# Optimization experiments

Measured on AMD Instinct MI355X. Metric: run time of the kernel, lower is better.

## Reference

```python
import jax, jax.numpy as jnp
import numpy as np

EPS = 1e-12  # torch F.normalize default eps

def _l2norm(x):
    # F.normalize(x, dim=1): x / max(||x||, eps)
    n = jnp.sqrt(jnp.sum(x * x, axis=1, keepdims=True))
    return x / jnp.maximum(n, EPS)

def setup_inputs() -> dict:
    key = jax.random.key(0)
    k1, k2 = jax.random.split(key)
    B, M, D = 4096, 8192, 1024
    query = jax.random.normal(k1, (B, D), dtype=jnp.float32)
    memory = jax.random.normal(k2, (M, D), dtype=jnp.float32)
    return {"query": query, "memory": memory}

def reference(query, memory):
    # memory buffer is normalized at construction time
    mem = _l2norm(memory)              # [M, D]
    q = _l2norm(query)                 # [B, D]
    sim = jnp.einsum('bd,md->bm', q, mem)          # [B, M] cosine similarity
    attn = jax.nn.softmax(sim, axis=1)             # [B, M]
    memory_features = jnp.einsum('bm,md->bd', attn, mem)  # [B, D]
    return (memory_features, attn)
```

## Files before the change

### kernel.cpp

```cpp
#include <hip/hip_runtime.h>
#include <stdint.h>

#define NB 4096
#define NM 8192
#define ND 1024

typedef __attribute__((ext_vector_type(8))) short bf16x8;
typedef __attribute__((ext_vector_type(4))) float f32x4;
typedef __attribute__((ext_vector_type(8))) unsigned short u16x8;

static __device__ __forceinline__ unsigned short f2bf(float f) {
  union { float f; uint32_t u; } v; v.f = f;
  uint32_t u = v.u;
  u += 0x7fffu + ((u >> 16) & 1u);
  return (unsigned short)(u >> 16);
}
static __device__ __forceinline__ float bf2f(unsigned short b) {
  union { uint32_t u; float f; } v; v.u = ((uint32_t)b) << 16; return v.f;
}

static __device__ __forceinline__ void gload_lds16(const void* g, void* l) {
  __builtin_amdgcn_global_load_lds(
      (__attribute__((address_space(1))) void*)g,
      (__attribute__((address_space(3))) void*)l, 16, 0, 0);
}

#define BAR()   __builtin_amdgcn_s_barrier()
#define LGKM0() asm volatile("s_waitcnt lgkmcnt(0)" ::: "memory")
#define VMC8()  asm volatile("s_waitcnt vmcnt(8)" ::: "memory")
#define VMC2()  asm volatile("s_waitcnt vmcnt(2)" ::: "memory")
#define VMC0()  asm volatile("s_waitcnt vmcnt(0)" ::: "memory")

__global__ void nrm_kernel(const float* __restrict__ x, unsigned short* __restrict__ out) {
  const int row = blockIdx.x, t = threadIdx.x;
  const float4 v = ((const float4*)(x + (size_t)row * ND))[t];
  float ss = v.x * v.x + v.y * v.y + v.z * v.z + v.w * v.w;
  #pragma unroll
  for (int o = 32; o > 0; o >>= 1) ss += __shfl_xor(ss, o);
  __shared__ float red[4];
  if ((t & 63) == 0) red[t >> 6] = ss;
  __syncthreads();
  ss = (red[0] + red[1]) + (red[2] + red[3]);
  const float sc = 1.0f / fmaxf(sqrtf(ss), 1e-12f);
  ushort4 o4;
  o4.x = f2bf(v.x * sc); o4.y = f2bf(v.y * sc);
  o4.z = f2bf(v.z * sc); o4.w = f2bf(v.w * sc);
  ((ushort4*)(out + (size_t)row * ND))[t] = o4;
}

__global__ void tr_kernel(const unsigned short* __restrict__ memn, unsigned short* __restrict__ memt) {
  __shared__ unsigned short Ts[64][66];
  const int t = threadIdx.x;
  const int d0 = blockIdx.x * 64, m0 = blockIdx.y * 64;
  #pragma unroll
  for (int r = 0; r < 2; ++r) {
    const int lrow = r * 32 + (t >> 3);
    const int lcol = (t & 7) * 8;
    u16x8 v = *(const u16x8*)(memn + (size_t)(m0 + lrow) * ND + d0 + lcol);
    #pragma unroll
    for (int j = 0; j < 8; ++j) Ts[lcol + j][lrow] = v[j];
  }
  __syncthreads();
  #pragma unroll
  for (int r = 0; r < 2; ++r) {
    const int orow = r * 32 + (t >> 3);
    const int ocol = (t & 7) * 8;
    u16x8 o;
    #pragma unroll
    for (int j = 0; j < 8; ++j) o[j] = Ts[orow][ocol + j];
    *(u16x8*)(memt + (size_t)(d0 + orow) * NM + m0 + ocol) = o;
  }
}

template<int MODE>
__global__ __launch_bounds__(512, 2) void gemm4r(
    const unsigned short* __restrict__ A, const unsigned short* __restrict__ B,
    void* __restrict__ Cv, float* __restrict__ psum,
    int ld, int ldc, int mt, int tps, int kchunk, unsigned long long cstride)
{
  extern __shared__ char smem[];
  const int t = threadIdx.x;
  const int w = t >> 6, l = t & 63;
  const int wr = w >> 2, wc = w & 3;
  const int nwg = gridDim.x, cpx = nwg >> 3;
  const int id = (blockIdx.x & 7) * cpx + (blockIdx.x >> 3);
  const int ksp = id / tps, rem = id % tps;
  const int brow = rem % mt, bcol = rem / mt;
  const int k0 = ksp * kchunk;
  const int nt = kchunk >> 6;

  const int srow = l >> 3;
  const int scol = ((l & 7) ^ srow) << 3;
  const int lr = l & 15, lhi = l >> 4;
  const int swz = (l & 7) << 4;
  const int cbk0 = (lhi * 16) ^ swz;
  const int cbk1 = (64 + lhi * 16) ^ swz;
  const int aoffr = (wr * 16 + lr) * 128;
  const int boffr = (wc * 16 + lr) * 128;

  const unsigned short* Ab = A + (size_t)(brow * 256 + w * 8 + srow) * ld + k0 + scol;
  const unsigned short* Bb = B + (size_t)(bcol * 256 + w * 8 + srow) * ld + k0 + scol;

  auto stageA = [&](int p, int h, int tau) {
    const int kt = (tau < nt ? tau : nt - 1) << 6;
    const unsigned short* g = Ab + (size_t)(h * 128) * ld + kt;
    char* d = smem + p * 65536 + h * 16384 + w * 1024;
    gload_lds16(g, d);
    gload_lds16(g + (size_t)64 * ld, d + 8192);
  };
  auto stageB = [&](int p, int h, int tau) {
    const int kt = (tau < nt ? tau : nt - 1) << 6;
    const unsigned short* g = Bb + (size_t)(h * 128) * ld + kt;
    char* d = smem + p * 65536 + 32768 + h * 16384 + w * 1024;
    gload_lds16(g, d);
    gload_lds16(g + (size_t)64 * ld, d + 8192);
  };
  auto ldA = [&](int p, int m, int kk) -> bf16x8 {
    return *(const bf16x8*)(smem + p * 65536 + m * 4096 + aoffr + (kk ? cbk1 : cbk0));
  };
  auto ldB = [&](int p, int nf, int kk) -> bf16x8 {
    return *(const bf16x8*)(smem + p * 65536 + 32768 + nf * 8192 + boffr + (kk ? cbk1 : cbk0));
  };

  f32x4 acc[8][4] = {};
  bf16x8 alo[4][2], ahi[4][2], bloA[2][2], bloB[2][2], bhi[2][2];

  stageA(0, 0, 0); stageA(0, 1, 0); stageB(0, 0, 0); stageB(0, 1, 0);
  stageA(1, 0, 1); stageA(1, 1, 1); stageB(1, 0, 1); stageB(1, 1, 1);
  VMC8();
  BAR();
  #pragma unroll
  for (int m = 0; m < 4; ++m) { alo[m][0] = ldA(0, m, 0); alo[m][1] = ldA(0, m, 1); }
  #pragma unroll
  for (int n = 0; n < 2; ++n) { bloA[n][0] = ldB(0, n, 0); bloA[n][1] = ldB(0, n, 1); }

  #define CL(AF, BF, MO, NO)                                                   \
    __builtin_amdgcn_s_setprio(1);                                             \
    _Pragma("unroll")                                                          \
    for (int kk = 0; kk < 2; ++kk)                                             \
      _Pragma("unroll")                                                        \
      for (int m = 0; m < 4; ++m)                                              \
        _Pragma("unroll")                                                      \
        for (int n = 0; n < 2; ++n)                                            \
          acc[MO + m][NO + n] = __builtin_amdgcn_mfma_f32_16x16x32_bf16(       \
              AF[m][kk], BF[n][kk], acc[MO + m][NO + n], 0, 0, 0);             \
    __builtin_amdgcn_s_setprio(0);

  const int niter = nt >> 1;
  for (int i = 0; i < niter; ++i) {
    const int t2 = 2 * i + 2, t3 = 2 * i + 3;
    LGKM0();
    CL(alo, bloA, 0, 0);
    #pragma unroll
    for (int n = 0; n < 2; ++n) { bhi[n][0] = ldB(0, 2 + n, 0); bhi[n][1] = ldB(0, 2 + n, 1); }
    BAR();
    LGKM0();
    CL(alo, bhi, 0, 2);
    #pragma unroll
    for (int m = 0; m < 4; ++m) { ahi[m][0] = ldA(0, 4 + m, 0); ahi[m][1] = ldA(0, 4 + m, 1); }
    stageB(0, 0, t2);
    VMC2();
    BAR();
    LGKM0();
    CL(ahi, bhi, 4, 2);
    #pragma unroll
    for (int n = 0; n < 2; ++n) { bloB[n][0] = ldB(1, n, 0); bloB[n][1] = ldB(1, n, 1); }
    stageB(0, 1, t2); stageA(0, 0, t2);
    BAR();
    LGKM0();
    CL(ahi, bloA, 4, 0);
    #pragma unroll
    for (int m = 0; m < 4; ++m) { alo[m][0] = ldA(1, m, 0); alo[m][1] = ldA(1, m, 1); }
    stageA(0, 1, t2);
    BAR();
    LGKM0();
    CL(alo, bloB, 0, 0);
    #pragma unroll
    for (int n = 0; n < 2; ++n) { bhi[n][0] = ldB(1, 2 + n, 0); bhi[n][1] = ldB(1, 2 + n, 1); }
    BAR();
    LGKM0();
    CL(alo, bhi, 0, 2);
    #pragma unroll
    for (int m = 0; m < 4; ++m) { ahi[m][0] = ldA(1, 4 + m, 0); ahi[m][1] = ldA(1, 4 + m, 1); }
    stageB(1, 0, t3);
    VMC2();
    BAR();
    LGKM0();
    CL(ahi, bhi, 4, 2);
    #pragma unroll
    for (int n = 0; n < 2; ++n) { bloA[n][0] = ldB(0, n, 0); bloA[n][1] = ldB(0, n, 1); }
    stageB(1, 1, t3); stageA(1, 0, t3);
    BAR();
    LGKM0();
    CL(ahi, bloB, 4, 0);
    #pragma unroll
    for (int m = 0; m < 4; ++m) { alo[m][0] = ldA(0, m, 0); alo[m][1] = ldA(0, m, 1); }
    stageA(1, 1, t3);
    BAR();
  }
  #undef CL

  const int crow0 = brow * 256 + wr * 16 + lhi * 4;
  const int ccol0 = bcol * 256 + wc * 16 + lr;
  if constexpr (MODE == 1) {
    unsigned short* Cp = (unsigned short*)Cv;
    float rs[8][4];
    #pragma unroll
    for (int m = 0; m < 8; ++m)
      #pragma unroll
      for (int j = 0; j < 4; ++j) rs[m][j] = 0.f;
    #pragma unroll
    for (int m = 0; m < 8; ++m)
      #pragma unroll
      for (int n = 0; n < 4; ++n)
        #pragma unroll
        for (int j = 0; j < 4; ++j) {
          const float e = __expf(acc[m][n][j]);
          rs[m][j] += e;
          Cp[(size_t)(crow0 + m * 32 + j) * ldc + ccol0 + n * 64] = f2bf(e);
        }
    #pragma unroll
    for (int m = 0; m < 8; ++m)
      #pragma unroll
      for (int j = 0; j < 4; ++j)
        #pragma unroll
        for (int o = 1; o < 16; o <<= 1) rs[m][j] += __shfl_xor(rs[m][j], o);
    VMC0();
    __syncthreads();
    float* ls = (float*)smem;
    if (lr == 0) {
      #pragma unroll
      for (int m = 0; m < 8; ++m)
        #pragma unroll
        for (int j = 0; j < 4; ++j)
          ls[wc * 256 + wr * 16 + m * 32 + lhi * 4 + j] = rs[m][j];
    }
    __syncthreads();
    if (t < 256) {
      const float s4 = ls[t] + ls[256 + t] + ls[512 + t] + ls[768 + t];
      psum[(size_t)bcol * NB + brow * 256 + t] = s4;
    }
  } else {
    float* Cp = (float*)Cv + (unsigned long long)ksp * cstride;
    #pragma unroll
    for (int m = 0; m < 8; ++m)
      #pragma unroll
      for (int n = 0; n < 4; ++n)
        #pragma unroll
        for (int j = 0; j < 4; ++j)
          Cp[(size_t)(crow0 + m * 32 + j) * ldc + ccol0 + n * 64] = acc[m][n][j];
  }
}

__global__ void scale_kernel(const unsigned short* __restrict__ E,
                             const float* __restrict__ psum,
                             float* __restrict__ attn, float* __restrict__ sinv) {
  const int row = blockIdx.x, t = threadIdx.x;
  __shared__ float sh;
  if (t < 64) {
    float p = (t < 32) ? psum[(size_t)t * NB + row] : 0.f;
    #pragma unroll
    for (int o = 16; o > 0; o >>= 1) p += __shfl_xor(p, o);
    if (t == 0) { sh = p; sinv[row] = 1.0f / p; }
  }
  __syncthreads();
  const float inv = 1.0f / sh;
  const unsigned short* erow = E + (size_t)row * NM;
  float* arow = attn + (size_t)row * NM;
  #pragma unroll
  for (int i = 0; i < 4; ++i) {
    u16x8 bv = ((const u16x8*)erow)[i * 256 + t];
    float4 f0, f1;
    #pragma unroll
    for (int j = 0; j < 8; ++j) {
      const float a = bf2f(bv[j]) * inv;
      if (j < 4) (&f0.x)[j] = a; else (&f1.x)[j - 4] = a;
    }
    const int e = (i * 256 + t) * 8;
    *(float4*)(arow + e) = f0;
    *(float4*)(arow + e + 4) = f1;
  }
}

__global__ void reduce_kernel(const float4* __restrict__ part, float4* __restrict__ mf,
                              const float* __restrict__ sinv) {
  const size_t n4 = (size_t)NB * ND / 4;
  for (size_t i = (size_t)blockIdx.x * blockDim.x + threadIdx.x; i < n4;
       i += (size_t)gridDim.x * blockDim.x) {
    const float is = sinv[i >> 8];
    float4 s = part[i];
    #pragma unroll
    for (int k = 1; k < 4; ++k) {
      float4 p = part[(size_t)k * n4 + i];
      s.x += p.x; s.y += p.y; s.z += p.z; s.w += p.w;
    }
    s.x *= is; s.y *= is; s.z *= is; s.w *= is;
    mf[i] = s;
  }
}

extern "C" void kernel_launch(void* const* d_in, const int* in_sizes, int n_in,
                              void* d_out, int out_size, void* d_ws, size_t ws_size,
                              hipStream_t stream) {
  const float* q   = (const float*)d_in[0];
  const float* mem = (const float*)d_in[1];
  float* mf   = (float*)d_out;
  float* attn = (float*)d_out + (size_t)NB * ND;
  char* ws = (char*)d_ws;
  unsigned short* qn   = (unsigned short*)(ws);
  unsigned short* memn = (unsigned short*)(ws + ((size_t)8  << 20));
  unsigned short* memt = (unsigned short*)(ws + ((size_t)24 << 20));
  unsigned short* E    = (unsigned short*)(ws + ((size_t)40 << 20));
  float* psum          = (float*)(ws + ((size_t)104 << 20));
  float* sinv          = (float*)(ws + ((size_t)104 << 20) + (512 << 10));
  float* part          = (float*)(ws + ((size_t)105 << 20));

  hipFuncSetAttribute((const void*)gemm4r<1>,
                      hipFuncAttributeMaxDynamicSharedMemorySize, 131072);
  hipFuncSetAttribute((const void*)gemm4r<0>,
                      hipFuncAttributeMaxDynamicSharedMemorySize, 131072);

  hipLaunchKernelGGL(nrm_kernel, dim3(NM), dim3(256), 0, stream, mem, memn);
  hipLaunchKernelGGL(nrm_kernel, dim3(NB), dim3(256), 0, stream, q, qn);
  hipLaunchKernelGGL(tr_kernel, dim3(ND / 64, NM / 64), dim3(256), 0, stream, memn, memt);

  hipLaunchKernelGGL((gemm4r<1>), dim3((NB / 256) * (NM / 256)), dim3(512), 131072, stream,
                     qn, memn, (void*)E, psum, ND, NM, NB / 256,
                     (NB / 256) * (NM / 256), ND, 0ULL);

  hipLaunchKernelGGL(scale_kernel, dim3(NB), dim3(256), 0, stream, E, psum, attn, sinv);

  const int tps = (NB / 256) * (ND / 256);
  hipLaunchKernelGGL((gemm4r<0>), dim3(tps * 4), dim3(512), 131072, stream,
                     E, memt, (void*)part, (float*)nullptr, NM, ND, NB / 256, tps, NM / 4,
                     (unsigned long long)NB * ND);
  hipLaunchKernelGGL(reduce_kernel, dim3(2048), dim3(256), 0, stream,
                     (const float4*)part, (float4*)mf, sinv);
}
```

Measured before the change: 208.3 us.

## Fuse attn scaling into second GEMM epilogue and restructure GEMM pipeline per tile

```diff
diff --git a/kernel.cpp b/kernel.cpp
--- a/kernel.cpp
+++ b/kernel.cpp
@@ -27,8 +27,8 @@
 
 #define BAR()   __builtin_amdgcn_s_barrier()
 #define LGKM0() asm volatile("s_waitcnt lgkmcnt(0)" ::: "memory")
-#define VMC8()  asm volatile("s_waitcnt vmcnt(8)" ::: "memory")
-#define VMC2()  asm volatile("s_waitcnt vmcnt(2)" ::: "memory")
+#define LGKM8() asm volatile("s_waitcnt lgkmcnt(8)" ::: "memory")
+#define VMC4()  asm volatile("s_waitcnt vmcnt(4)" ::: "memory")
 #define VMC0()  asm volatile("s_waitcnt vmcnt(0)" ::: "memory")
 
 __global__ void nrm_kernel(const float* __restrict__ x, unsigned short* __restrict__ out) {
@@ -73,9 +73,10 @@
 }
 
 template<int MODE>
-__global__ __launch_bounds__(512, 2) void gemm4r(
+__global__ __launch_bounds__(512, 2) void gemmht(
     const unsigned short* __restrict__ A, const unsigned short* __restrict__ B,
     void* __restrict__ Cv, float* __restrict__ psum,
+    const float* __restrict__ sinvp, float* __restrict__ attnp,
     int ld, int ldc, int mt, int tps, int kchunk, unsigned long long cstride)
 {
   extern __shared__ char smem[];
@@ -123,16 +124,7 @@
   };
 
   f32x4 acc[8][4] = {};
-  bf16x8 alo[4][2], ahi[4][2], bloA[2][2], bloB[2][2], bhi[2][2];
-
-  stageA(0, 0, 0); stageA(0, 1, 0); stageB(0, 0, 0); stageB(0, 1, 0);
-  stageA(1, 0, 1); stageA(1, 1, 1); stageB(1, 0, 1); stageB(1, 1, 1);
-  VMC8();
-  BAR();
-  #pragma unroll
-  for (int m = 0; m < 4; ++m) { alo[m][0] = ldA(0, m, 0); alo[m][1] = ldA(0, m, 1); }
-  #pragma unroll
-  for (int n = 0; n < 2; ++n) { bloA[n][0] = ldB(0, n, 0); bloA[n][1] = ldB(0, n, 1); }
+  bf16x8 alo[4][2], ahi[4][2], blo[2][2], bhi[2][2];
 
   #define CL(AF, BF, MO, NO)                                                   \
     __builtin_amdgcn_s_setprio(1);                                             \
@@ -146,57 +138,45 @@
               AF[m][kk], BF[n][kk], acc[MO + m][NO + n], 0, 0, 0);             \
     __builtin_amdgcn_s_setprio(0);
 
+  stageA(0, 0, 0); stageB(0, 0, 0); stageB(0, 1, 0); stageA(0, 1, 0);
+  VMC4();
+  BAR();
+
+  auto tile_body = [&](int p, int q, int tau) {
+    #pragma unroll
+    for (int m = 0; m < 4; ++m) { alo[m][0] = ldA(p, m, 0); alo[m][1] = ldA(p, m, 1); }
+    #pragma unroll
+    for (int n = 0; n < 2; ++n) { blo[n][0] = ldB(p, n, 0); blo[n][1] = ldB(p, n, 1); }
+    stageA(q, 0, tau);
+    LGKM8();
+    BAR(); LGKM0();
+    CL(alo, blo, 0, 0);
+    VMC4();
+    BAR();
+    #pragma unroll
+    for (int n = 0; n < 2; ++n) { bhi[n][0] = ldB(p, 2 + n, 0); bhi[n][1] = ldB(p, 2 + n, 1); }
+    stageB(q, 0, tau);
+    BAR(); LGKM0();
+    CL(alo, bhi, 0, 2);
+    VMC4();
+    BAR();
+    #pragma unroll
+    for (int m = 0; m < 4; ++m) { ahi[m][0] = ldA(p, 4 + m, 0); ahi[m][1] = ldA(p, 4 + m, 1); }
+    stageB(q, 1, tau);
+    BAR(); LGKM0();
+    CL(ahi, bhi, 4, 2);
+    BAR();
+    stageA(q, 1, tau);
+    BAR();
+    CL(ahi, blo, 4, 0);
+    VMC4();
+    BAR();
+  };
+
   const int niter = nt >> 1;
   for (int i = 0; i < niter; ++i) {
-    const int t2 = 2 * i + 2, t3 = 2 * i + 3;
-    LGKM0();
-    CL(alo, bloA, 0, 0);
-    #pragma unroll
-    for (int n = 0; n < 2; ++n) { bhi[n][0] = ldB(0, 2 + n, 0); bhi[n][1] = ldB(0, 2 + n, 1); }
-    BAR();
-    LGKM0();
-    CL(alo, bhi, 0, 2);
-    #pragma unroll
-    for (int m = 0; m < 4; ++m) { ahi[m][0] = ldA(0, 4 + m, 0); ahi[m][1] = ldA(0, 4 + m, 1); }
-    stageB(0, 0, t2);
-    VMC2();
-    BAR();
-    LGKM0();
-    CL(ahi, bhi, 4, 2);
-    #pragma unroll
-    for (int n = 0; n < 2; ++n) { bloB[n][0] = ldB(1, n, 0); bloB[n][1] = ldB(1, n, 1); }
-    stageB(0, 1, t2); stageA(0, 0, t2);
-    BAR();
-    LGKM0();
-    CL(ahi, bloA, 4, 0);
-    #pragma unroll
-    for (int m = 0; m < 4; ++m) { alo[m][0] = ldA(1, m, 0); alo[m][1] = ldA(1, m, 1); }
-    stageA(0, 1, t2);
-    BAR();
-    LGKM0();
-    CL(alo, bloB, 0, 0);
-    #pragma unroll
-    for (int n = 0; n < 2; ++n) { bhi[n][0] = ldB(1, 2 + n, 0); bhi[n][1] = ldB(1, 2 + n, 1); }
-    BAR();
-    LGKM0();
-    CL(alo, bhi, 0, 2);
-    #pragma unroll
-    for (int m = 0; m < 4; ++m) { ahi[m][0] = ldA(1, 4 + m, 0); ahi[m][1] = ldA(1, 4 + m, 1); }
-    stageB(1, 0, t3);
-    VMC2();
-    BAR();
-    LGKM0();
-    CL(ahi, bhi, 4, 2);
-    #pragma unroll
-    for (int n = 0; n < 2; ++n) { bloA[n][0] = ldB(0, n, 0); bloA[n][1] = ldB(0, n, 1); }
-    stageB(1, 1, t3); stageA(1, 0, t3);
-    BAR();
-    LGKM0();
-    CL(ahi, bloB, 4, 0);
-    #pragma unroll
-    for (int m = 0; m < 4; ++m) { alo[m][0] = ldA(0, m, 0); alo[m][1] = ldA(0, m, 1); }
-    stageA(1, 1, t3);
-    BAR();
+    tile_body(0, 1, 2 * i + 1);
+    tile_body(1, 0, 2 * i + 2);
   }
   #undef CL
 
@@ -249,37 +229,34 @@
         #pragma unroll
         for (int j = 0; j < 4; ++j)
           Cp[(size_t)(crow0 + m * 32 + j) * ldc + ccol0 + n * 64] = acc[m][n][j];
-  }
-}
-
-__global__ void scale_kernel(const unsigned short* __restrict__ E,
-                             const float* __restrict__ psum,
-                             float* __restrict__ attn, float* __restrict__ sinv) {
-  const int row = blockIdx.x, t = threadIdx.x;
-  __shared__ float sh;
-  if (t < 64) {
-    float p = (t < 32) ? psum[(size_t)t * NB + row] : 0.f;
-    #pragma unroll
-    for (int o = 16; o > 0; o >>= 1) p += __shfl_xor(p, o);
-    if (t == 0) { sh = p; sinv[row] = 1.0f / p; }
-  }
-  __syncthreads();
-  const float inv = 1.0f / sh;
-  const unsigned short* erow = E + (size_t)row * NM;
-  float* arow = attn + (size_t)row * NM;
+    if (sinvp != nullptr) {
+      const int r0 = brow * 256 + bcol * 64;
+      const unsigned short* Ea = A;
+      const int nch = kchunk >> 3;
+      for (int idx = t; idx < 64 * nch; idx += 512) {
+        const int row = idx / nch, ch = idx % nch;
+        const float inv = sinvp[r0 + row];
+        u16x8 bv = *(const u16x8*)(Ea + (size_t)(r0 + row) * ld + k0 + ch * 8);
+        float4 f0, f1;
+        #pragma unroll
+        for (int j = 0; j < 8; ++j) {
+          const float a = bf2f(bv[j]) * inv;
+          if (j < 4) (&f0.x)[j] = a; else (&f1.x)[j - 4] = a;
+        }
+        float* arow = attnp + (size_t)(r0 + row) * NM + k0 + ch * 8;
+        *(float4*)arow = f0;
+        *(float4*)(arow + 4) = f1;
+      }
+    }
+  }
+}
+
+__global__ void sinv_kernel(const float* __restrict__ psum, float* __restrict__ sinv) {
+  const int row = blockIdx.x * 256 + threadIdx.x;
+  float s = 0.f;
   #pragma unroll
-  for (int i = 0; i < 4; ++i) {
-    u16x8 bv = ((const u16x8*)erow)[i * 256 + t];
-    float4 f0, f1;
-    #pragma unroll
-    for (int j = 0; j < 8; ++j) {
-      const float a = bf2f(bv[j]) * inv;
-      if (j < 4) (&f0.x)[j] = a; else (&f1.x)[j - 4] = a;
-    }
-    const int e = (i * 256 + t) * 8;
-    *(float4*)(arow + e) = f0;
-    *(float4*)(arow + e + 4) = f1;
-  }
+  for (int k = 0; k < 32; ++k) s += psum[(size_t)k * NB + row];
+  sinv[row] = 1.0f / s;
 }
 
 __global__ void reduce_kernel(const float4* __restrict__ part, float4* __restrict__ mf,
@@ -315,25 +292,25 @@
   float* sinv          = (float*)(ws + ((size_t)104 << 20) + (512 << 10));
   float* part          = (float*)(ws + ((size_t)105 << 20));
 
-  hipFuncSetAttribute((const void*)gemm4r<1>,
+  hipFuncSetAttribute((const void*)gemmht<1>,
                       hipFuncAttributeMaxDynamicSharedMemorySize, 131072);
-  hipFuncSetAttribute((const void*)gemm4r<0>,
+  hipFuncSetAttribute((const void*)gemmht<0>,
                       hipFuncAttributeMaxDynamicSharedMemorySize, 131072);
 
   hipLaunchKernelGGL(nrm_kernel, dim3(NM), dim3(256), 0, stream, mem, memn);
   hipLaunchKernelGGL(nrm_kernel, dim3(NB), dim3(256), 0, stream, q, qn);
   hipLaunchKernelGGL(tr_kernel, dim3(ND / 64, NM / 64), dim3(256), 0, stream, memn, memt);
 
-  hipLaunchKernelGGL((gemm4r<1>), dim3((NB / 256) * (NM / 256)), dim3(512), 131072, stream,
-                     qn, memn, (void*)E, psum, ND, NM, NB / 256,
-                     (NB / 256) * (NM / 256), ND, 0ULL);
-
-  hipLaunchKernelGGL(scale_kernel, dim3(NB), dim3(256), 0, stream, E, psum, attn, sinv);
+  hipLaunchKernelGGL((gemmht<1>), dim3((NB / 256) * (NM / 256)), dim3(512), 131072, stream,
+                     qn, memn, (void*)E, psum, (const float*)nullptr, (float*)nullptr,
+                     ND, NM, NB / 256, (NB / 256) * (NM / 256), ND, 0ULL);
+
+  hipLaunchKernelGGL(sinv_kernel, dim3(NB / 256), dim3(256), 0, stream, psum, sinv);
 
   const int tps = (NB / 256) * (ND / 256);
-  hipLaunchKernelGGL((gemm4r<0>), dim3(tps * 4), dim3(512), 131072, stream,
-                     E, memt, (void*)part, (float*)nullptr, NM, ND, NB / 256, tps, NM / 4,
-                     (unsigned long long)NB * ND);
+  hipLaunchKernelGGL((gemmht<0>), dim3(tps * 4), dim3(512), 131072, stream,
+                     E, memt, (void*)part, (float*)nullptr, sinv, attn,
+                     NM, ND, NB / 256, tps, NM / 4, (unsigned long long)NB * ND);
   hipLaunchKernelGGL(reduce_kernel, dim3(2048), dim3(256), 0, stream,
                      (const float4*)part, (float4*)mf, sinv);
 }
```

Measured after the change: 219.9 us. 5.6% more time.

## Restructure GEMM main loop into per-tile body with partial LDS waits

Applied to the files above, without the earlier changes.

```diff
diff --git a/kernel.cpp b/kernel.cpp
--- a/kernel.cpp
+++ b/kernel.cpp
@@ -26,9 +26,9 @@
 }
 
 #define BAR()   __builtin_amdgcn_s_barrier()
-#define LGKM0() asm volatile("s_waitcnt lgkmcnt(0)" ::: "memory")
+#define LGKM8() asm volatile("s_waitcnt lgkmcnt(8)" ::: "memory")
+#define LGKM4() asm volatile("s_waitcnt lgkmcnt(4)" ::: "memory")
 #define VMC8()  asm volatile("s_waitcnt vmcnt(8)" ::: "memory")
-#define VMC2()  asm volatile("s_waitcnt vmcnt(2)" ::: "memory")
 #define VMC0()  asm volatile("s_waitcnt vmcnt(0)" ::: "memory")
 
 __global__ void nrm_kernel(const float* __restrict__ x, unsigned short* __restrict__ out) {
@@ -73,7 +73,7 @@
 }
 
 template<int MODE>
-__global__ __launch_bounds__(512, 2) void gemm4r(
+__global__ __launch_bounds__(512, 2) void gemmcl(
     const unsigned short* __restrict__ A, const unsigned short* __restrict__ B,
     void* __restrict__ Cv, float* __restrict__ psum,
     int ld, int ldc, int mt, int tps, int kchunk, unsigned long long cstride)
@@ -123,16 +123,7 @@
   };
 
   f32x4 acc[8][4] = {};
-  bf16x8 alo[4][2], ahi[4][2], bloA[2][2], bloB[2][2], bhi[2][2];
-
-  stageA(0, 0, 0); stageA(0, 1, 0); stageB(0, 0, 0); stageB(0, 1, 0);
-  stageA(1, 0, 1); stageA(1, 1, 1); stageB(1, 0, 1); stageB(1, 1, 1);
-  VMC8();
-  BAR();
-  #pragma unroll
-  for (int m = 0; m < 4; ++m) { alo[m][0] = ldA(0, m, 0); alo[m][1] = ldA(0, m, 1); }
-  #pragma unroll
-  for (int n = 0; n < 2; ++n) { bloA[n][0] = ldB(0, n, 0); bloA[n][1] = ldB(0, n, 1); }
+  bf16x8 a0[4][2], a1[4][2], b0[2][2], b1[2][2];
 
   #define CL(AF, BF, MO, NO)                                                   \
     __builtin_amdgcn_s_setprio(1);                                             \
@@ -146,57 +137,47 @@
               AF[m][kk], BF[n][kk], acc[MO + m][NO + n], 0, 0, 0);             \
     __builtin_amdgcn_s_setprio(0);
 
+  stageA(0, 0, 0); stageB(0, 0, 0); stageA(0, 1, 0); stageB(0, 1, 0);
+  stageA(1, 0, 1); stageB(1, 0, 1); stageA(1, 1, 1); stageB(1, 1, 1);
+  VMC8();
+  BAR();
+  #pragma unroll
+  for (int m = 0; m < 4; ++m) { a0[m][0] = ldA(0, m, 0); a0[m][1] = ldA(0, m, 1); }
+  #pragma unroll
+  for (int n = 0; n < 2; ++n) { b0[n][0] = ldB(0, n, 0); b0[n][1] = ldB(0, n, 1); }
+
+  auto tile_body = [&](int p, int q, int tau2) {
+    #pragma unroll
+    for (int m = 0; m < 4; ++m) { a1[m][0] = ldA(p, 4 + m, 0); a1[m][1] = ldA(p, 4 + m, 1); }
+    BAR(); LGKM8();
+    CL(a0, b0, 0, 0);
+    BAR();
+    #pragma unroll
+    for (int n = 0; n < 2; ++n) { b1[n][0] = ldB(p, 2 + n, 0); b1[n][1] = ldB(p, 2 + n, 1); }
+    stageA(p, 0, tau2); stageB(p, 0, tau2);
+    BAR(); LGKM4();
+    CL(a1, b0, 4, 0);
+    VMC8();
+    BAR();
+    #pragma unroll
+    for (int n = 0; n < 2; ++n) { b0[n][0] = ldB(q, n, 0); b0[n][1] = ldB(q, n, 1); }
+    stageA(p, 1, tau2);
+    BAR(); LGKM4();
+    CL(a1, b1, 4, 2);
+    BAR();
+    stageB(p, 1, tau2);
+    BAR();
+    CL(a0, b1, 0, 2);
+    #pragma unroll
+    for (int m = 0; m < 4; ++m) { a0[m][0] = ldA(q, m, 0); a0[m][1] = ldA(q, m, 1); }
+    VMC8();
+    BAR();
+  };
+
   const int niter = nt >> 1;
   for (int i = 0; i < niter; ++i) {
-    const int t2 = 2 * i + 2, t3 = 2 * i + 3;
-    LGKM0();
-    CL(alo, bloA, 0, 0);
-    #pragma unroll
-    for (int n = 0; n < 2; ++n) { bhi[n][0] = ldB(0, 2 + n, 0); bhi[n][1] = ldB(0, 2 + n, 1); }
-    BAR();
-    LGKM0();
-    CL(alo, bhi, 0, 2);
-    #pragma unroll
-    for (int m = 0; m < 4; ++m) { ahi[m][0] = ldA(0, 4 + m, 0); ahi[m][1] = ldA(0, 4 + m, 1); }
-    stageB(0, 0, t2);
-    VMC2();
-    BAR();
-    LGKM0();
-    CL(ahi, bhi, 4, 2);
-    #pragma unroll
-    for (int n = 0; n < 2; ++n) { bloB[n][0] = ldB(1, n, 0); bloB[n][1] = ldB(1, n, 1); }
-    stageB(0, 1, t2); stageA(0, 0, t2);
-    BAR();
-    LGKM0();
-    CL(ahi, bloA, 4, 0);
-    #pragma unroll
-    for (int m = 0; m < 4; ++m) { alo[m][0] = ldA(1, m, 0); alo[m][1] = ldA(1, m, 1); }
-    stageA(0, 1, t2);
-    BAR();
-    LGKM0();
-    CL(alo, bloB, 0, 0);
-    #pragma unroll
-    for (int n = 0; n < 2; ++n) { bhi[n][0] = ldB(1, 2 + n, 0); bhi[n][1] = ldB(1, 2 + n, 1); }
-    BAR();
-    LGKM0();
-    CL(alo, bhi, 0, 2);
-    #pragma unroll
-    for (int m = 0; m < 4; ++m) { ahi[m][0] = ldA(1, 4 + m, 0); ahi[m][1] = ldA(1, 4 + m, 1); }
-    stageB(1, 0, t3);
-    VMC2();
-    BAR();
-    LGKM0();
-    CL(ahi, bhi, 4, 2);
-    #pragma unroll
-    for (int n = 0; n < 2; ++n) { bloA[n][0] = ldB(0, n, 0); bloA[n][1] = ldB(0, n, 1); }
-    stageB(1, 1, t3); stageA(1, 0, t3);
-    BAR();
-    LGKM0();
-    CL(ahi, bloB, 4, 0);
-    #pragma unroll
-    for (int m = 0; m < 4; ++m) { alo[m][0] = ldA(0, m, 0); alo[m][1] = ldA(0, m, 1); }
-    stageA(1, 1, t3);
-    BAR();
+    tile_body(0, 1, 2 * i + 2);
+    tile_body(1, 0, 2 * i + 3);
   }
   #undef CL
 
@@ -315,23 +296,23 @@
   float* sinv          = (float*)(ws + ((size_t)104 << 20) + (512 << 10));
   float* part          = (float*)(ws + ((size_t)105 << 20));
 
-  hipFuncSetAttribute((const void*)gemm4r<1>,
+  hipFuncSetAttribute((const void*)gemmcl<1>,
                       hipFuncAttributeMaxDynamicSharedMemorySize, 131072);
-  hipFuncSetAttribute((const void*)gemm4r<0>,
+  hipFuncSetAttribute((const void*)gemmcl<0>,
                       hipFuncAttributeMaxDynamicSharedMemorySize, 131072);
 
   hipLaunchKernelGGL(nrm_kernel, dim3(NM), dim3(256), 0, stream, mem, memn);
   hipLaunchKernelGGL(nrm_kernel, dim3(NB), dim3(256), 0, stream, q, qn);
   hipLaunchKernelGGL(tr_kernel, dim3(ND / 64, NM / 64), dim3(256), 0, stream, memn, memt);
 
-  hipLaunchKernelGGL((gemm4r<1>), dim3((NB / 256) * (NM / 256)), dim3(512), 131072, stream,
+  hipLaunchKernelGGL((gemmcl<1>), dim3((NB / 256) * (NM / 256)), dim3(512), 131072, stream,
                      qn, memn, (void*)E, psum, ND, NM, NB / 256,
                      (NB / 256) * (NM / 256), ND, 0ULL);
 
   hipLaunchKernelGGL(scale_kernel, dim3(NB), dim3(256), 0, stream, E, psum, attn, sinv);
 
   const int tps = (NB / 256) * (ND / 256);
-  hipLaunchKernelGGL((gemm4r<0>), dim3(tps * 4), dim3(512), 131072, stream,
+  hipLaunchKernelGGL((gemmcl<0>), dim3(tps * 4), dim3(512), 131072, stream,
                      E, memt, (void*)part, (float*)nullptr, NM, ND, NB / 256, tps, NM / 4,
                      (unsigned long long)NB * ND);
   hipLaunchKernelGGL(reduce_kernel, dim3(2048), dim3(256), 0, stream,
```

Measured after the change: 241.4 us. 15.9% more time.

## Compute similarity GEMM in FP8 with MX-scaled MFMA instead of bf16

Applied to the files above, without the earlier changes.

```diff
diff --git a/kernel.cpp b/kernel.cpp
--- a/kernel.cpp
+++ b/kernel.cpp
@@ -8,6 +8,10 @@
 typedef __attribute__((ext_vector_type(8))) short bf16x8;
 typedef __attribute__((ext_vector_type(4))) float f32x4;
 typedef __attribute__((ext_vector_type(8))) unsigned short u16x8;
+typedef __attribute__((ext_vector_type(4))) int i32x4;
+typedef __attribute__((ext_vector_type(8))) int i32x8;
+
+#define SCONE 0x7F7F7F7F
 
 static __device__ __forceinline__ unsigned short f2bf(float f) {
   union { float f; uint32_t u; } v; v.f = f;
@@ -18,6 +22,24 @@
 static __device__ __forceinline__ float bf2f(unsigned short b) {
   union { uint32_t u; float f; } v; v.u = ((uint32_t)b) << 16; return v.f;
 }
+static __device__ __forceinline__ uint8_t f2fp8(float f) {
+  union { float f; uint32_t u; } v; v.f = f;
+  const uint8_t s = (uint8_t)((v.u >> 31) << 7);
+  const float a = fabsf(f);
+  if (a >= 448.f) return s | 0x7E;
+  if (a < 0.0009765625f) return s;
+  const uint32_t u = v.u & 0x7FFFFFFFu;
+  const int e = (int)(u >> 23) - 127;
+  if (e < -6) {
+    int m = (int)rintf(a * 512.f);
+    if (m >= 8) return s | 0x08;
+    return s | (uint8_t)m;
+  }
+  const uint32_t r = u + 0x7FFFFu + ((u >> 20) & 1u);
+  const int e2 = (int)(r >> 23) - 127;
+  if (e2 > 8) return s | 0x7E;
+  return s | (uint8_t)((e2 + 7) << 3) | (uint8_t)((r >> 20) & 7u);
+}
 
 static __device__ __forceinline__ void gload_lds16(const void* g, void* l) {
   __builtin_amdgcn_global_load_lds(
@@ -31,7 +53,8 @@
 #define VMC2()  asm volatile("s_waitcnt vmcnt(2)" ::: "memory")
 #define VMC0()  asm volatile("s_waitcnt vmcnt(0)" ::: "memory")
 
-__global__ void nrm_kernel(const float* __restrict__ x, unsigned short* __restrict__ out) {
+__global__ void nrm_m8(const float* __restrict__ x, unsigned short* __restrict__ ob,
+                       uint8_t* __restrict__ o8) {
   const int row = blockIdx.x, t = threadIdx.x;
   const float4 v = ((const float4*)(x + (size_t)row * ND))[t];
   float ss = v.x * v.x + v.y * v.y + v.z * v.z + v.w * v.w;
@@ -45,7 +68,28 @@
   ushort4 o4;
   o4.x = f2bf(v.x * sc); o4.y = f2bf(v.y * sc);
   o4.z = f2bf(v.z * sc); o4.w = f2bf(v.w * sc);
-  ((ushort4*)(out + (size_t)row * ND))[t] = o4;
+  ((ushort4*)(ob + (size_t)row * ND))[t] = o4;
+  uchar4 c4;
+  c4.x = f2fp8(v.x * sc); c4.y = f2fp8(v.y * sc);
+  c4.z = f2fp8(v.z * sc); c4.w = f2fp8(v.w * sc);
+  ((uchar4*)(o8 + (size_t)row * ND))[t] = c4;
+}
+
+__global__ void nrm_q8(const float* __restrict__ x, uint8_t* __restrict__ o8) {
+  const int row = blockIdx.x, t = threadIdx.x;
+  const float4 v = ((const float4*)(x + (size_t)row * ND))[t];
+  float ss = v.x * v.x + v.y * v.y + v.z * v.z + v.w * v.w;
+  #pragma unroll
+  for (int o = 32; o > 0; o >>= 1) ss += __shfl_xor(ss, o);
+  __shared__ float red[4];
+  if ((t & 63) == 0) red[t >> 6] = ss;
+  __syncthreads();
+  ss = (red[0] + red[1]) + (red[2] + red[3]);
+  const float sc = 1.0f / fmaxf(sqrtf(ss), 1e-12f);
+  uchar4 c4;
+  c4.x = f2fp8(v.x * sc); c4.y = f2fp8(v.y * sc);
+  c4.z = f2fp8(v.z * sc); c4.w = f2fp8(v.w * sc);
+  ((uchar4*)(o8 + (size_t)row * ND))[t] = c4;
 }
 
 __global__ void tr_kernel(const unsigned short* __restrict__ memn, unsigned short* __restrict__ memt) {
@@ -72,11 +116,179 @@
   }
 }
 
-template<int MODE>
+__global__ __launch_bounds__(512, 2) void gemm4x(
+    const uint8_t* __restrict__ A, const uint8_t* __restrict__ B,
+    unsigned short* __restrict__ E, float* __restrict__ psum,
+    int ld, int ldc, int mt, int kchunk)
+{
+  extern __shared__ char smem[];
+  const int t = threadIdx.x;
+  const int w = t >> 6, l = t & 63;
+  const int wr = w >> 2, wc = w & 3;
+  const int nwg = gridDim.x, cpx = nwg >> 3;
+  const int id = (blockIdx.x & 7) * cpx + (blockIdx.x >> 3);
+  const int brow = id % mt, bcol = id / mt;
+  const int nt = kchunk >> 7;
+
+  const int srow = l >> 3;
+  const int scol = ((l & 7) ^ srow) << 4;
+  const int lr = l & 15, lhi = l >> 4;
+  const int swz = (l & 7) << 4;
+  const int cb0 = (lhi * 32) ^ swz;
+  const int cb1 = (lhi * 32 + 16) ^ swz;
+  const int aoffr = (wr * 16 + lr) * 128;
+  const int boffr = (wc * 16 + lr) * 128;
+
+  const uint8_t* Ab = A + (size_t)(brow * 256 + w * 8 + srow) * ld + scol;
+  const uint8_t* Bb = B + (size_t)(bcol * 256 + w * 8 + srow) * ld + scol;
+
+  auto stageA = [&](int p, int h, int tau) {
+    const int kt = (tau < nt ? tau : nt - 1) << 7;
+    const uint8_t* g = Ab + (size_t)(h * 128) * ld + kt;
+    char* d = smem + p * 65536 + h * 16384 + w * 1024;
+    gload_lds16(g, d);
+    gload_lds16(g + (size_t)64 * ld, d + 8192);
+  };
+  auto stageB = [&](int p, int h, int tau) {
+    const int kt = (tau < nt ? tau : nt - 1) << 7;
+    const uint8_t* g = Bb + (size_t)(h * 128) * ld + kt;
+    char* d = smem + p * 65536 + 32768 + h * 16384 + w * 1024;
+    gload_lds16(g, d);
+    gload_lds16(g + (size_t)64 * ld, d + 8192);
+  };
+  auto ldA4 = [&](int p, int m, int c) -> i32x4 {
+    return *(const i32x4*)(smem + p * 65536 + m * 4096 + aoffr + (c ? cb1 : cb0));
+  };
+  auto ldB4 = [&](int p, int nf, int c) -> i32x4 {
+    return *(const i32x4*)(smem + p * 65536 + 32768 + nf * 8192 + boffr + (c ? cb1 : cb0));
+  };
+
+  f32x4 acc[8][4] = {};
+  i32x8 alo[4], ahi[4], bloA[2], bloB[2], bhi[2];
+
+  #define RDA4(DST, P, MB)                                                     \
+    _Pragma("unroll")                                                          \
+    for (int m_ = 0; m_ < 4; ++m_) {                                           \
+      i32x4 lo_ = ldA4(P, (MB) + m_, 0), hi_ = ldA4(P, (MB) + m_, 1);          \
+      i32x8 r_; r_[0]=lo_[0]; r_[1]=lo_[1]; r_[2]=lo_[2]; r_[3]=lo_[3];        \
+      r_[4]=hi_[0]; r_[5]=hi_[1]; r_[6]=hi_[2]; r_[7]=hi_[3]; DST[m_] = r_; }
+  #define RDB4(DST, P, NBASE)                                                  \
+    _Pragma("unroll")                                                          \
+    for (int n_ = 0; n_ < 2; ++n_) {                                           \
+      i32x4 lo_ = ldB4(P, (NBASE) + n_, 0), hi_ = ldB4(P, (NBASE) + n_, 1);    \
+      i32x8 r_; r_[0]=lo_[0]; r_[1]=lo_[1]; r_[2]=lo_[2]; r_[3]=lo_[3];        \
+      r_[4]=hi_[0]; r_[5]=hi_[1]; r_[6]=hi_[2]; r_[7]=hi_[3]; DST[n_] = r_; }
+  #define CL8(AF, BF, MO, NO)                                                  \
+    __builtin_amdgcn_s_setprio(1);                                             \
+    _Pragma("unroll")                                                          \
+    for (int m_ = 0; m_ < 4; ++m_)                                             \
+      _Pragma("unroll")                                                        \
+      for (int n_ = 0; n_ < 2; ++n_)                                           \
+        acc[(MO) + m_][(NO) + n_] =                                            \
+            __builtin_amdgcn_mfma_scale_f32_16x16x128_f8f6f4(                  \
+                AF[m_], BF[n_], acc[(MO) + m_][(NO) + n_],                     \
+                0, 0, 0, SCONE, 0, SCONE);                                     \
+    __builtin_amdgcn_s_setprio(0);
+
+  stageA(0, 0, 0); stageA(0, 1, 0); stageB(0, 0, 0); stageB(0, 1, 0);
+  stageA(1, 0, 1); stageA(1, 1, 1); stageB(1, 0, 1); stageB(1, 1, 1);
+  VMC8();
+  BAR();
+  RDA4(alo, 0, 0);
+  RDB4(bloA, 0, 0);
+
+  const int niter = nt >> 1;
+  for (int i = 0; i < niter; ++i) {
+    const int t2 = 2 * i + 2, t3 = 2 * i + 3;
+    LGKM0();
+    CL8(alo, bloA, 0, 0);
+    RDB4(bhi, 0, 2);
+    BAR();
+    LGKM0();
+    CL8(alo, bhi, 0, 2);
+    RDA4(ahi, 0, 4);
+    stageB(0, 0, t2);
+    VMC2();
+    BAR();
+    LGKM0();
+    CL8(ahi, bhi, 4, 2);
+    RDB4(bloB, 1, 0);
+    stageB(0, 1, t2); stageA(0, 0, t2);
+    BAR();
+    LGKM0();
+    CL8(ahi, bloA, 4, 0);
+    RDA4(alo, 1, 0);
+    stageA(0, 1, t2);
+    BAR();
+    LGKM0();
+    CL8(alo, bloB, 0, 0);
+    RDB4(bhi, 1, 2);
+    BAR();
+    LGKM0();
+    CL8(alo, bhi, 0, 2);
+    RDA4(ahi, 1, 4);
+    stageB(1, 0, t3);
+    VMC2();
+    BAR();
+    LGKM0();
+    CL8(ahi, bhi, 4, 2);
+    RDB4(bloA, 0, 0);
+    stageB(1, 1, t3); stageA(1, 0, t3);
+    BAR();
+    LGKM0();
+    CL8(ahi, bloB, 4, 0);
+    RDA4(alo, 0, 0);
+    stageA(1, 1, t3);
+    BAR();
+  }
+  #undef RDA4
+  #undef RDB4
+  #undef CL8
+
+  const int crow0 = brow * 256 + wr * 16 + lhi * 4;
+  const int ccol0 = bcol * 256 + wc * 16 + lr;
+  float rs[8][4];
+  #pragma unroll
+  for (int m = 0; m < 8; ++m)
+    #pragma unroll
+    for (int j = 0; j < 4; ++j) rs[m][j] = 0.f;
+  #pragma unroll
+  for (int m = 0; m < 8; ++m)
+    #pragma unroll
+    for (int n = 0; n < 4; ++n)
+      #pragma unroll
+      for (int j = 0; j < 4; ++j) {
+        const float e = __expf(acc[m][n][j]);
+        rs[m][j] += e;
+        E[(size_t)(crow0 + m * 32 + j) * ldc + ccol0 + n * 64] = f2bf(e);
+      }
+  #pragma unroll
+  for (int m = 0; m < 8; ++m)
+    #pragma unroll
+    for (int j = 0; j < 4; ++j)
+      #pragma unroll
+      for (int o = 1; o < 16; o <<= 1) rs[m][j] += __shfl_xor(rs[m][j], o);
+  VMC0();
+  __syncthreads();
+  float* ls = (float*)smem;
+  if (lr == 0) {
+    #pragma unroll
+    for (int m = 0; m < 8; ++m)
+      #pragma unroll
+      for (int j = 0; j < 4; ++j)
+        ls[wc * 256 + wr * 16 + m * 32 + lhi * 4 + j] = rs[m][j];
+  }
+  __syncthreads();
+  if (t < 256) {
+    const float s4 = ls[t] + ls[256 + t] + ls[512 + t] + ls[768 + t];
+    psum[(size_t)bcol * NB + brow * 256 + t] = s4;
+  }
+}
+
 __global__ __launch_bounds__(512, 2) void gemm4r(
     const unsigned short* __restrict__ A, const unsigned short* __restrict__ B,
-    void* __restrict__ Cv, float* __restrict__ psum,
-    int ld, int ldc, int mt, int tps, int kchunk, unsigned long long cstride)
+    float* __restrict__ C, int ld, int ldc, int mt, int tps, int kchunk,
+    unsigned long long cstride)
 {
   extern __shared__ char smem[];
   const int t = threadIdx.x;
@@ -202,54 +414,14 @@
 
   const int crow0 = brow * 256 + wr * 16 + lhi * 4;
   const int ccol0 = bcol * 256 + wc * 16 + lr;
-  if constexpr (MODE == 1) {
-    unsigned short* Cp = (unsigned short*)Cv;
-    float rs[8][4];
-    #pragma unroll
-    for (int m = 0; m < 8; ++m)
-      #pragma unroll
-      for (int j = 0; j < 4; ++j) rs[m][j] = 0.f;
-    #pragma unroll
-    for (int m = 0; m < 8; ++m)
-      #pragma unroll
-      for (int n = 0; n < 4; ++n)
-        #pragma unroll
-        for (int j = 0; j < 4; ++j) {
-          const float e = __expf(acc[m][n][j]);
-          rs[m][j] += e;
-          Cp[(size_t)(crow0 + m * 32 + j) * ldc + ccol0 + n * 64] = f2bf(e);
-        }
-    #pragma unroll
-    for (int m = 0; m < 8; ++m)
+  float* Cp = C + (unsigned long long)ksp * cstride;
+  #pragma unroll
+  for (int m = 0; m < 8; ++m)
+    #pragma unroll
+    for (int n = 0; n < 4; ++n)
       #pragma unroll
       for (int j = 0; j < 4; ++j)
-        #pragma unroll
-        for (int o = 1; o < 16; o <<= 1) rs[m][j] += __shfl_xor(rs[m][j], o);
-    VMC0();
-    __syncthreads();
-    float* ls = (float*)smem;
-    if (lr == 0) {
-      #pragma unroll
-      for (int m = 0; m < 8; ++m)
-        #pragma unroll
-        for (int j = 0; j < 4; ++j)
-          ls[wc * 256 + wr * 16 + m * 32 + lhi * 4 + j] = rs[m][j];
-    }
-    __syncthreads();
-    if (t < 256) {
-      const float s4 = ls[t] + ls[256 + t] + ls[512 + t] + ls[768 + t];
-      psum[(size_t)bcol * NB + brow * 256 + t] = s4;
-    }
-  } else {
-    float* Cp = (float*)Cv + (unsigned long long)ksp * cstride;
-    #pragma unroll
-    for (int m = 0; m < 8; ++m)
-      #pragma unroll
-      for (int n = 0; n < 4; ++n)
-        #pragma unroll
-        for (int j = 0; j < 4; ++j)
-          Cp[(size_t)(crow0 + m * 32 + j) * ldc + ccol0 + n * 64] = acc[m][n][j];
-  }
+        Cp[(size_t)(crow0 + m * 32 + j) * ldc + ccol0 + n * 64] = acc[m][n][j];
 }
 
 __global__ void scale_kernel(const unsigned short* __restrict__ E,
@@ -307,32 +479,32 @@
   float* mf   = (float*)d_out;
   float* attn = (float*)d_out + (size_t)NB * ND;
   char* ws = (char*)d_ws;
-  unsigned short* qn   = (unsigned short*)(ws);
+  uint8_t* memn8       = (uint8_t*)(ws);
   unsigned short* memn = (unsigned short*)(ws + ((size_t)8  << 20));
   unsigned short* memt = (unsigned short*)(ws + ((size_t)24 << 20));
   unsigned short* E    = (unsigned short*)(ws + ((size_t)40 << 20));
   float* psum          = (float*)(ws + ((size_t)104 << 20));
   float* sinv          = (float*)(ws + ((size_t)104 << 20) + (512 << 10));
   float* part          = (float*)(ws + ((size_t)105 << 20));
-
-  hipFuncSetAttribute((const void*)gemm4r<1>,
+  uint8_t* qn8         = (uint8_t*)(ws + ((size_t)105 << 20));
+
+  hipFuncSetAttribute((const void*)gemm4x,
                       hipFuncAttributeMaxDynamicSharedMemorySize, 131072);
-  hipFuncSetAttribute((const void*)gemm4r<0>,
+  hipFuncSetAttribute((const void*)gemm4r,
                       hipFuncAttributeMaxDynamicSharedMemorySize, 131072);
 
-  hipLaunchKernelGGL(nrm_kernel, dim3(NM), dim3(256), 0, stream, mem, memn);
-  hipLaunchKernelGGL(nrm_kernel, dim3(NB), dim3(256), 0, stream, q, qn);
+  hipLaunchKernelGGL(nrm_m8, dim3(NM), dim3(256), 0, stream, mem, memn, memn8);
+  hipLaunchKernelGGL(nrm_q8, dim3(NB), dim3(256), 0, stream, q, qn8);
   hipLaunchKernelGGL(tr_kernel, dim3(ND / 64, NM / 64), dim3(256), 0, stream, memn, memt);
 
-  hipLaunchKernelGGL((gemm4r<1>), dim3((NB / 256) * (NM / 256)), dim3(512), 131072, stream,
-                     qn, memn, (void*)E, psum, ND, NM, NB / 256,
-                     (NB / 256) * (NM / 256), ND, 0ULL);
+  hipLaunchKernelGGL(gemm4x, dim3((NB / 256) * (NM / 256)), dim3(512), 131072, stream,
+                     qn8, memn8, E, psum, ND, NM, NB / 256, ND);
 
   hipLaunchKernelGGL(scale_kernel, dim3(NB), dim3(256), 0, stream, E, psum, attn, sinv);
 
   const int tps = (NB / 256) * (ND / 256);
-  hipLaunchKernelGGL((gemm4r<0>), dim3(tps * 4), dim3(512), 131072, stream,
-                     E, memt, (void*)part, (float*)nullptr, NM, ND, NB / 256, tps, NM / 4,
+  hipLaunchKernelGGL(gemm4r, dim3(tps * 4), dim3(512), 131072, stream,
+                     E, memt, part, NM, ND, NB / 256, tps, NM / 4,
                      (unsigned long long)NB * ND);
   hipLaunchKernelGGL(reduce_kernel, dim3(2048), dim3(256), 0, stream,
                      (const float4*)part, (float4*)mf, sinv);
```

New measurement: 187.2 us. 1.11x faster.
